# Kernel optimization log

Measured on AMD Instinct MI355X. Metric: run time of the kernel, lower is better.

Reference implementation:

```python
import jax, jax.numpy as jnp
import numpy as np


def setup_inputs() -> dict:
    key = jax.random.key(0)
    k1, k2, k3, k4 = jax.random.split(key, 4)
    B, N, d_in, d_out = 8, 2048, 256, 256
    x = jax.random.normal(k1, (B, N, d_in), dtype=jnp.float32)
    adj_hat = jax.random.uniform(k2, (B, N, N), dtype=jnp.float32)
    W = jax.random.normal(k3, (d_out, d_in), dtype=jnp.float32) * (1.0 / np.sqrt(d_in))
    b = jax.random.normal(k4, (d_out,), dtype=jnp.float32) * 0.01
    return {"x": x, "adj_hat": adj_hat, "W": W, "b": b}


def reference(x, adj_hat, W, b):
    # Degrees from adj = adj_hat - I (i.e. without self loops): row sum minus diagonal.
    N = adj_hat.shape[1]
    diag = jnp.diagonal(adj_hat, axis1=-2, axis2=-1)          # [B, N]
    d = adj_hat.sum(axis=-1) - diag                           # [B, N]
    d_inv_sqrt = jnp.power(d, -0.5)                           # [B, N]
    # dad = D^-1/2 @ adj_hat @ D^-1/2  ==  d_i * a_ij * d_j (elementwise broadcast)
    dad = d_inv_sqrt[:, :, None] * adj_hat * d_inv_sqrt[:, None, :]  # [B, N, N]
    h = jnp.einsum('bnd,od->bno', x, W) + b                   # projection [B, N, d_out]
    return jnp.einsum('bnm,bmo->bno', dad, h)                 # [B, N, d_out]
```

## Files before the change

### kernel.cpp

```cpp
#include <hip/hip_runtime.h>
#include <hip/hip_bf16.h>


#define BATCH 8
#define NN    2048
#define DIN   256
#define DOUT  256
#define RTOT  (BATCH * NN)
#define HP    (RTOT + 32)

typedef short  bf16x8  __attribute__((ext_vector_type(8)));
typedef short  short4v __attribute__((ext_vector_type(4)));
typedef float  f32x4   __attribute__((ext_vector_type(4)));

__device__ __forceinline__ short f2bf(float f) {
    union { float f; unsigned u; } v; v.f = f;
    unsigned r = v.u + 0x7fffu + ((v.u >> 16) & 1u);
    return (short)(r >> 16);
}

__device__ __forceinline__ void gl_lds16(const unsigned short* g, unsigned short* l) {
    __builtin_amdgcn_global_load_lds(
        (const __attribute__((address_space(1))) unsigned int*)g,
        (__attribute__((address_space(3))) unsigned int*)l, 16, 0, 0);
}

__global__ __launch_bounds__(256) void k_degree(const float* __restrict__ adj,
                                                float* __restrict__ dis) {
    const int row = blockIdx.x;
    const int n = row & (NN - 1);
    const int tid = threadIdx.x;
    const float4* rp4 = (const float4*)(adj + (size_t)row * NN);

    float s = 0.f;
#pragma unroll
    for (int i = 0; i < 2; i++) {
        float4 v = rp4[tid + i * 256];
        s += (v.x + v.y) + (v.z + v.w);
    }
#pragma unroll
    for (int off = 32; off; off >>= 1) s += __shfl_down(s, off);
    __shared__ float red[4];
    if ((tid & 63) == 0) red[tid >> 6] = s;
    __syncthreads();
    if (tid == 0) {
        float tot  = (red[0] + red[1]) + (red[2] + red[3]);
        float diag = ((const float*)rp4)[n];
        dis[row]   = rsqrtf(tot - diag);
    }
}

__global__ __launch_bounds__(256) void k_proj(const float* __restrict__ x,
                                              const float* __restrict__ W,
                                              const float* __restrict__ bias,
                                              const float* __restrict__ dis,
                                              unsigned short* __restrict__ hT) {
    const int mt  = blockIdx.y;
    const int nt  = blockIdx.x;
    const int tid = threadIdx.x;
    const int w = tid >> 6, lane = tid & 63;
    const int wr = w >> 1, wc = w & 1;
    const int l16 = lane & 15, quad = lane >> 4;

    __shared__ short As[128][32];
    __shared__ short Bs[128][32];

    f32x4 acc[4][4];
#pragma unroll
    for (int i = 0; i < 4; i++)
#pragma unroll
        for (int j = 0; j < 4; j++) acc[i][j] = (f32x4){0.f, 0.f, 0.f, 0.f};

    const float4* Wf4 = (const float4*)(W + (size_t)mt * 128 * DIN);
    const float4* Xf4 = (const float4*)(x + (size_t)nt * 128 * DIN);

    for (int kk = 0; kk < DIN / 32; kk++) {
        const int k0 = kk * 32;
        __syncthreads();
#pragma unroll
        for (int it = 0; it < 4; it++) {
            int idx = tid + it * 256;
            int r = idx >> 3, c = idx & 7;
            float4 va = Wf4[(size_t)r * (DIN / 4) + (k0 >> 2) + c];
            float4 vb = Xf4[(size_t)r * (DIN / 4) + (k0 >> 2) + c];
            short4v sa = { f2bf(va.x), f2bf(va.y), f2bf(va.z), f2bf(va.w) };
            short4v sb = { f2bf(vb.x), f2bf(vb.y), f2bf(vb.z), f2bf(vb.w) };
            *(short4v*)&As[r][c * 4] = sa;
            *(short4v*)&Bs[r][c * 4] = sb;
        }
        __syncthreads();
        bf16x8 af[4], bfv[4];
#pragma unroll
        for (int i = 0; i < 4; i++) af[i]  = *(bf16x8*)&As[wr * 64 + i * 16 + l16][quad * 8];
#pragma unroll
        for (int j = 0; j < 4; j++) bfv[j] = *(bf16x8*)&Bs[wc * 64 + j * 16 + l16][quad * 8];
#pragma unroll
        for (int i = 0; i < 4; i++)
#pragma unroll
            for (int j = 0; j < 4; j++)
                acc[i][j] = __builtin_amdgcn_mfma_f32_16x16x32_bf16(af[i], bfv[j], acc[i][j], 0, 0, 0);
    }

#pragma unroll
    for (int i = 0; i < 4; i++) {
        const int orow_base = mt * 128 + wr * 64 + i * 16 + quad * 4;
#pragma unroll
        for (int r = 0; r < 4; r++) {
            const int orow = orow_base + r;
            const float bb = bias[orow];
#pragma unroll
            for (int j = 0; j < 4; j++) {
                const int col = nt * 128 + wc * 64 + j * 16 + l16;
                float v = (acc[i][j][r] + bb) * dis[col];
                hT[(size_t)orow * HP + col] = (unsigned short)f2bf(v);
            }
        }
    }
}

__global__ __launch_bounds__(256, 2) void k_main(const float* __restrict__ adj,
                                                 const unsigned short* __restrict__ hT,
                                                 const float* __restrict__ dis,
                                                 float* __restrict__ out) {
    const int bx    = blockIdx.x;
    const int b     = bx & 7;
    const int mtile = (bx >> 3) & 31;
    const int ctile = bx >> 8;
    const int n0    = mtile * 64;
    const int tid  = threadIdx.x;
    const int w    = tid >> 6, lane = tid & 63;
    const int l16  = lane & 15, quad = lane >> 4;
    const int lr   = lane >> 2;
    const int lc   = (lane & 3) * 8;

    __shared__ short As[4][64][32];
    __shared__ short Bs[4][128][32];

    const float4* agf4 = (const float4*)(adj + (size_t)(b * NN + n0 + w * 16 + lr) * NN + lc);
    const unsigned short* bgp0 = hT + (size_t)(ctile * 128 + w * 32 + lr) * HP + b * NN + lc;
    const unsigned short* bgp1 = bgp0 + (size_t)16 * HP;

    f32x4 acc[4][2];
#pragma unroll
    for (int i = 0; i < 4; i++)
#pragma unroll
        for (int j = 0; j < 2; j++) acc[i][j] = (f32x4){0.f, 0.f, 0.f, 0.f};

    for (int g = 0; g < NN / 128; g++) {
#pragma unroll
        for (int s = 0; s < 4; s++) {
            const int ko = g * 128 + s * 32;
            gl_lds16(bgp0 + ko, (unsigned short*)&Bs[s][w * 32][0]);
            gl_lds16(bgp1 + ko, (unsigned short*)&Bs[s][w * 32 + 16][0]);
        }
        float4 av0[4], av1[4];
#pragma unroll
        for (int s = 0; s < 4; s++) {
            av0[s] = agf4[g * 32 + s * 8];
            av1[s] = agf4[g * 32 + s * 8 + 1];
        }
#pragma unroll
        for (int s = 0; s < 4; s++) {
            bf16x8 pk = { f2bf(av0[s].x), f2bf(av0[s].y), f2bf(av0[s].z), f2bf(av0[s].w),
                          f2bf(av1[s].x), f2bf(av1[s].y), f2bf(av1[s].z), f2bf(av1[s].w) };
            *(bf16x8*)&As[s][w * 16 + lr][lc] = pk;
        }
        __syncthreads();
#pragma unroll
        for (int s = 0; s < 4; s++) {
            bf16x8 af[4], bfv[2];
#pragma unroll
            for (int i = 0; i < 4; i++) af[i]  = *(bf16x8*)&As[s][i * 16 + l16][quad * 8];
#pragma unroll
            for (int j = 0; j < 2; j++) bfv[j] = *(bf16x8*)&Bs[s][w * 32 + j * 16 + l16][quad * 8];
#pragma unroll
            for (int i = 0; i < 4; i++)
#pragma unroll
                for (int j = 0; j < 2; j++)
                    acc[i][j] = __builtin_amdgcn_mfma_f32_16x16x32_bf16(af[i], bfv[j], acc[i][j], 0, 0, 0);
        }
        __syncthreads();
    }

    const float* disb = dis + (size_t)b * NN;
#pragma unroll
    for (int i = 0; i < 4; i++) {
#pragma unroll
        for (int r = 0; r < 4; r++) {
            const int nrow = n0 + i * 16 + quad * 4 + r;
            const float dn = disb[nrow];
#pragma unroll
            for (int j = 0; j < 2; j++) {
                const int ocol = ctile * 128 + w * 32 + j * 16 + l16;
                out[((size_t)b * NN + nrow) * DOUT + ocol] = dn * acc[i][j][r];
            }
        }
    }
}

extern "C" void kernel_launch(void* const* d_in, const int* in_sizes, int n_in,
                              void* d_out, int out_size, void* d_ws, size_t ws_size,
                              hipStream_t stream) {
    const float* x    = (const float*)d_in[0];
    const float* adj  = (const float*)d_in[1];
    const float* W    = (const float*)d_in[2];
    const float* bias = (const float*)d_in[3];
    float* out = (float*)d_out;

    float* dis = (float*)d_ws;
    unsigned short* hT  = (unsigned short*)((char*)d_ws + 65536);

    k_degree<<<RTOT, 256, 0, stream>>>(adj, dis);
    k_proj<<<dim3(128, 2), 256, 0, stream>>>(x, W, bias, dis, hT);
    k_main<<<512, 256, 0, stream>>>(adj, hT, dis, out);
}
```

Before: 254.0 us.

## Merge degree and projection kernels; apply column scaling to adjacency in main

The degree reduction and the x·W projection now run in one launch, with projection blocks first and row-degree blocks after, so the two can overlap. This removes the dependency that made the projection wait for dis. The per-column D^-1/2 scaling moves out of the projection epilogue and into the main kernel, where each adjacency value is multiplied by dis[m] before conversion to bf16. The cost is extra dis loads and multiplies in k_main's inner loop, and a larger grid for the merged kernel.

Result: faster. 244.6 us, median of 2 (-3.7%).

```diff
diff --git a/kernel.cpp b/kernel.cpp
--- a/kernel.cpp
+++ b/kernel.cpp
@@ -25,95 +25,96 @@
         (__attribute__((address_space(3))) unsigned int*)l, 16, 0, 0);
 }
 
-__global__ __launch_bounds__(256) void k_degree(const float* __restrict__ adj,
-                                                float* __restrict__ dis) {
-    const int row = blockIdx.x;
-    const int n = row & (NN - 1);
+__global__ __launch_bounds__(256) void k_deg_proj(const float* __restrict__ adj,
+                                                  const float* __restrict__ x,
+                                                  const float* __restrict__ W,
+                                                  const float* __restrict__ bias,
+                                                  float* __restrict__ dis,
+                                                  unsigned short* __restrict__ hT) {
     const int tid = threadIdx.x;
-    const float4* rp4 = (const float4*)(adj + (size_t)row * NN);
-
-    float s = 0.f;
-#pragma unroll
-    for (int i = 0; i < 2; i++) {
-        float4 v = rp4[tid + i * 256];
-        s += (v.x + v.y) + (v.z + v.w);
-    }
-#pragma unroll
-    for (int off = 32; off; off >>= 1) s += __shfl_down(s, off);
-    __shared__ float red[4];
-    if ((tid & 63) == 0) red[tid >> 6] = s;
-    __syncthreads();
-    if (tid == 0) {
-        float tot  = (red[0] + red[1]) + (red[2] + red[3]);
-        float diag = ((const float*)rp4)[n];
-        dis[row]   = rsqrtf(tot - diag);
-    }
-}
-
-__global__ __launch_bounds__(256) void k_proj(const float* __restrict__ x,
-                                              const float* __restrict__ W,
-                                              const float* __restrict__ bias,
-                                              const float* __restrict__ dis,
-                                              unsigned short* __restrict__ hT) {
-    const int mt  = blockIdx.y;
-    const int nt  = blockIdx.x;
-    const int tid = threadIdx.x;
-    const int w = tid >> 6, lane = tid & 63;
-    const int wr = w >> 1, wc = w & 1;
-    const int l16 = lane & 15, quad = lane >> 4;
-
-    __shared__ short As[128][32];
-    __shared__ short Bs[128][32];
-
-    f32x4 acc[4][4];
-#pragma unroll
-    for (int i = 0; i < 4; i++)
-#pragma unroll
-        for (int j = 0; j < 4; j++) acc[i][j] = (f32x4){0.f, 0.f, 0.f, 0.f};
-
-    const float4* Wf4 = (const float4*)(W + (size_t)mt * 128 * DIN);
-    const float4* Xf4 = (const float4*)(x + (size_t)nt * 128 * DIN);
-
-    for (int kk = 0; kk < DIN / 32; kk++) {
-        const int k0 = kk * 32;
+
+    if (blockIdx.x < 256) {
+        const int bid = blockIdx.x;
+        const int mt  = bid >> 7;
+        const int nt  = bid & 127;
+        const int w = tid >> 6, lane = tid & 63;
+        const int wr = w >> 1, wc = w & 1;
+        const int l16 = lane & 15, quad = lane >> 4;
+
+        __shared__ short As[128][32];
+        __shared__ short Bs[128][32];
+
+        f32x4 acc[4][4];
+#pragma unroll
+        for (int i = 0; i < 4; i++)
+#pragma unroll
+            for (int j = 0; j < 4; j++) acc[i][j] = (f32x4){0.f, 0.f, 0.f, 0.f};
+
+        const float4* Wf4 = (const float4*)(W + (size_t)mt * 128 * DIN);
+        const float4* Xf4 = (const float4*)(x + (size_t)nt * 128 * DIN);
+
+        for (int kk = 0; kk < DIN / 32; kk++) {
+            const int k0 = kk * 32;
+            __syncthreads();
+#pragma unroll
+            for (int it = 0; it < 4; it++) {
+                int idx = tid + it * 256;
+                int r = idx >> 3, c = idx & 7;
+                float4 va = Wf4[(size_t)r * (DIN / 4) + (k0 >> 2) + c];
+                float4 vb = Xf4[(size_t)r * (DIN / 4) + (k0 >> 2) + c];
+                short4v sa = { f2bf(va.x), f2bf(va.y), f2bf(va.z), f2bf(va.w) };
+                short4v sb = { f2bf(vb.x), f2bf(vb.y), f2bf(vb.z), f2bf(vb.w) };
+                *(short4v*)&As[r][c * 4] = sa;
+                *(short4v*)&Bs[r][c * 4] = sb;
+            }
+            __syncthreads();
+            bf16x8 af[4], bfv[4];
+#pragma unroll
+            for (int i = 0; i < 4; i++) af[i]  = *(bf16x8*)&As[wr * 64 + i * 16 + l16][quad * 8];
+#pragma unroll
+            for (int j = 0; j < 4; j++) bfv[j] = *(bf16x8*)&Bs[wc * 64 + j * 16 + l16][quad * 8];
+#pragma unroll
+            for (int i = 0; i < 4; i++)
+#pragma unroll
+                for (int j = 0; j < 4; j++)
+                    acc[i][j] = __builtin_amdgcn_mfma_f32_16x16x32_bf16(af[i], bfv[j], acc[i][j], 0, 0, 0);
+        }
+
+#pragma unroll
+        for (int i = 0; i < 4; i++) {
+            const int orow_base = mt * 128 + wr * 64 + i * 16 + quad * 4;
+#pragma unroll
+            for (int r = 0; r < 4; r++) {
+                const int orow = orow_base + r;
+                const float bb = bias[orow];
+#pragma unroll
+                for (int j = 0; j < 4; j++) {
+                    const int col = nt * 128 + wc * 64 + j * 16 + l16;
+                    float v = acc[i][j][r] + bb;
+                    hT[(size_t)orow * HP + col] = (unsigned short)f2bf(v);
+                }
+            }
+        }
+    } else {
+        const int row = blockIdx.x - 256;
+        const int n = row & (NN - 1);
+        const float4* rp4 = (const float4*)(adj + (size_t)row * NN);
+
+        float s = 0.f;
+#pragma unroll
+        for (int i = 0; i < 2; i++) {
+            float4 v = rp4[tid + i * 256];
+            s += (v.x + v.y) + (v.z + v.w);
+        }
+#pragma unroll
+        for (int off = 32; off; off >>= 1) s += __shfl_down(s, off);
+        __shared__ float red[4];
+        if ((tid & 63) == 0) red[tid >> 6] = s;
         __syncthreads();
-#pragma unroll
-        for (int it = 0; it < 4; it++) {
-            int idx = tid + it * 256;
-            int r = idx >> 3, c = idx & 7;
-            float4 va = Wf4[(size_t)r * (DIN / 4) + (k0 >> 2) + c];
-            float4 vb = Xf4[(size_t)r * (DIN / 4) + (k0 >> 2) + c];
-            short4v sa = { f2bf(va.x), f2bf(va.y), f2bf(va.z), f2bf(va.w) };
-            short4v sb = { f2bf(vb.x), f2bf(vb.y), f2bf(vb.z), f2bf(vb.w) };
-            *(short4v*)&As[r][c * 4] = sa;
-            *(short4v*)&Bs[r][c * 4] = sb;
-        }
-        __syncthreads();
-        bf16x8 af[4], bfv[4];
-#pragma unroll
-        for (int i = 0; i < 4; i++) af[i]  = *(bf16x8*)&As[wr * 64 + i * 16 + l16][quad * 8];
-#pragma unroll
-        for (int j = 0; j < 4; j++) bfv[j] = *(bf16x8*)&Bs[wc * 64 + j * 16 + l16][quad * 8];
-#pragma unroll
-        for (int i = 0; i < 4; i++)
-#pragma unroll
-            for (int j = 0; j < 4; j++)
-                acc[i][j] = __builtin_amdgcn_mfma_f32_16x16x32_bf16(af[i], bfv[j], acc[i][j], 0, 0, 0);
-    }
-
-#pragma unroll
-    for (int i = 0; i < 4; i++) {
-        const int orow_base = mt * 128 + wr * 64 + i * 16 + quad * 4;
-#pragma unroll
-        for (int r = 0; r < 4; r++) {
-            const int orow = orow_base + r;
-            const float bb = bias[orow];
-#pragma unroll
-            for (int j = 0; j < 4; j++) {
-                const int col = nt * 128 + wc * 64 + j * 16 + l16;
-                float v = (acc[i][j][r] + bb) * dis[col];
-                hT[(size_t)orow * HP + col] = (unsigned short)f2bf(v);
-            }
+        if (tid == 0) {
+            float tot  = (red[0] + red[1]) + (red[2] + red[3]);
+            float diag = ((const float*)rp4)[n];
+            dis[row]   = rsqrtf(tot - diag);
         }
     }
 }
@@ -136,6 +137,7 @@
     __shared__ short As[4][64][32];
     __shared__ short Bs[4][128][32];
 
+    const float* disb = dis + (size_t)b * NN;
     const float4* agf4 = (const float4*)(adj + (size_t)(b * NN + n0 + w * 16 + lr) * NN + lc);
     const unsigned short* bgp0 = hT + (size_t)(ctile * 128 + w * 32 + lr) * HP + b * NN + lc;
     const unsigned short* bgp1 = bgp0 + (size_t)16 * HP;
@@ -161,8 +163,13 @@
         }
 #pragma unroll
         for (int s = 0; s < 4; s++) {
-            bf16x8 pk = { f2bf(av0[s].x), f2bf(av0[s].y), f2bf(av0[s].z), f2bf(av0[s].w),
-                          f2bf(av1[s].x), f2bf(av1[s].y), f2bf(av1[s].z), f2bf(av1[s].w) };
+            const float* dp = disb + g * 128 + s * 32 + lc;
+            float4 dv0 = *(const float4*)dp;
+            float4 dv1 = *(const float4*)(dp + 4);
+            bf16x8 pk = { f2bf(av0[s].x * dv0.x), f2bf(av0[s].y * dv0.y),
+                          f2bf(av0[s].z * dv0.z), f2bf(av0[s].w * dv0.w),
+                          f2bf(av1[s].x * dv1.x), f2bf(av1[s].y * dv1.y),
+                          f2bf(av1[s].z * dv1.z), f2bf(av1[s].w * dv1.w) };
             *(bf16x8*)&As[s][w * 16 + lr][lc] = pk;
         }
         __syncthreads();
@@ -182,7 +189,6 @@
         __syncthreads();
     }
 
-    const float* disb = dis + (size_t)b * NN;
 #pragma unroll
     for (int i = 0; i < 4; i++) {
 #pragma unroll
@@ -210,7 +216,6 @@
     float* dis = (float*)d_ws;
     unsigned short* hT  = (unsigned short*)((char*)d_ws + 65536);
 
-    k_degree<<<RTOT, 256, 0, stream>>>(adj, dis);
-    k_proj<<<dim3(128, 2), 256, 0, stream>>>(x, W, bias, dis, hT);
+    k_deg_proj<<<256 + RTOT, 256, 0, stream>>>(adj, x, W, bias, dis, hT);
     k_main<<<512, 256, 0, stream>>>(adj, hT, dis, out);
 }
```
